# Kernel tuning notes

Measured on AMD Instinct MI355X. Metric: run time of the kernel, lower is better.

The kernel has to match this reference:

```python
import jax, jax.numpy as jnp
import numpy as np


def _segmented_exclusive_cumsum(vals, seg_start_flags):
    """Exclusive cumsum of vals that resets at segment starts (flags True)."""
    def combine(a, b):
        va, fa = a
        vb, fb = b
        return (jnp.where(fb, vb, va + vb), fa | fb)
    inclusive, _ = jax.lax.associative_scan(combine, (vals, seg_start_flags))
    return inclusive - vals


def setup_inputs() -> dict:
    key = jax.random.key(0)
    k1, k2 = jax.random.split(key)
    n_rays = 65536
    samples_per_ray = 128  # average; ragged via sorted random ray ids
    n_pts = n_rays * samples_per_ray  # 8_388_608 sample points
    density = jax.random.normal(k1, (n_pts,), dtype=jnp.float32)
    ray_id = jnp.sort(jax.random.randint(k2, (n_pts,), 0, n_rays)).astype(jnp.int32)
    shift = jnp.float32(-3.0)      # self.act_shift
    interval = jnp.float32(0.5)    # stepsize * voxel_size_ratio
    return {"density": density, "shift": shift, "interval": interval,
            "ray_id": ray_id, "n_rays": n_rays}


def reference(density, shift, interval, ray_id, n_rays):
    # Raw2Alpha: alpha = 1 - exp(-softplus(density + shift) * interval)
    # log(1 - alpha) = -interval * softplus(density + shift)  (stable, no log of tiny)
    log_one_minus_alpha = -interval * jax.nn.softplus(density + shift)
    alpha = 1.0 - jnp.exp(log_one_minus_alpha)

    # Alphas2Weights: per-ray exclusive cumprod of (1 - alpha) in log space.
    # ray_id is sorted; segment starts where the ray id changes.
    seg_start = jnp.concatenate(
        [jnp.ones((1,), dtype=bool), ray_id[1:] != ray_id[:-1]])
    log_T = _segmented_exclusive_cumsum(log_one_minus_alpha, seg_start)
    T = jnp.exp(log_T)                      # transmittance before each sample
    weights = alpha * T                     # [n_pts]

    # alphainv_last[r] = prod over ray r of (1 - alpha) = residual transmittance
    log_total = jax.ops.segment_sum(log_one_minus_alpha, ray_id,
                                    num_segments=n_rays)
    alphainv_last = jnp.exp(log_total)      # [n_rays]; empty rays -> exp(0)=1
    return weights, alphainv_last
```

## Files before the change

kernel.cpp:

```cpp
#include <hip/hip_runtime.h>
#include <math.h>


#define LOG2E 1.4426950408889634f

typedef float vf4 __attribute__((ext_vector_type(4)));

__device__ __forceinline__ float exp2f_(float x) { return __builtin_amdgcn_exp2f(x); }
__device__ __forceinline__ float log2f_(float x) { return __builtin_amdgcn_logf(x); }
__device__ __forceinline__ float rsqf_(float x)  { return __builtin_amdgcn_rsqf(x); }

__device__ __forceinline__ float oma(float d, float sh2, float negc, bool fast) {
    const float y = fmaf(d, LOG2E, sh2);
    if (fast) return rsqf_(1.0f + exp2f_(y));
    const float sp = fmaxf(y, 0.f) + log2f_(1.f + exp2f_(-fabsf(y)));
    return exp2f_(negc * sp);
}

template <int CTRL, int RM>
__device__ __forceinline__ void seg_step(float& V, int& F) {
    const int vs_i = __builtin_amdgcn_update_dpp(
        0x3f800000, __builtin_bit_cast(int, V), CTRL, RM, 0xF, false);
    const int fs = __builtin_amdgcn_update_dpp(0, F, CTRL, RM, 0xF, false);
    const float vs = __builtin_bit_cast(float, vs_i);
    V = F ? V : vs * V;
    F = F | fs;
}

__device__ __forceinline__ float wave_prod_bcast(float x) {
#define STEPP(CTRL, RM)                                                        \
    { int t_ = __builtin_amdgcn_update_dpp(0x3f800000,                         \
          __builtin_bit_cast(int, x), CTRL, RM, 0xF, false);                   \
      x *= __builtin_bit_cast(float, t_); }
    STEPP(0x111, 0xF) STEPP(0x112, 0xF) STEPP(0x114, 0xF)
    STEPP(0x118, 0xF) STEPP(0x142, 0xA) STEPP(0x143, 0xC)
#undef STEPP
    return __builtin_bit_cast(float,
        __builtin_amdgcn_readlane(__builtin_bit_cast(int, x), 63));
}

__device__ __forceinline__ int wave_imax_bcast(int x) {
#define STEPM(CTRL, RM)                                                        \
    { int t_ = __builtin_amdgcn_update_dpp((int)0x80000000, x, CTRL, RM,       \
                                           0xF, false);                        \
      x = (x > t_) ? x : t_; }
    STEPM(0x111, 0xF) STEPM(0x112, 0xF) STEPM(0x114, 0xF)
    STEPM(0x118, 0xF) STEPM(0x142, 0xA) STEPM(0x143, 0xC)
#undef STEPM
    return __builtin_amdgcn_readlane(x, 63);
}

__global__ void __launch_bounds__(256)
fused_alpha_weights(const float* __restrict__ density,
                    const int*   __restrict__ ray_id,
                    const float* __restrict__ shift_p,
                    const float* __restrict__ interval_p,
                    float* __restrict__ weights,
                    float* __restrict__ alphainv,
                    int n_pts, int n_rays) {
    __shared__ float s_wv[4];
    __shared__ int   s_wf[4];
    __shared__ float s_red[4];
    __shared__ int   s_redi[4];

    const int t    = threadIdx.x;
    const int lane = t & 63;
    const int wid  = t >> 6;
    const int base = blockIdx.x << 10;
    const int idx0 = base + t * 4;

    const float shift = shift_p[0];
    const float c     = interval_p[0];
    const float sh2   = shift * LOG2E;
    const float negc  = -c;
    const bool  fast  = (c == 0.5f);

    int r[5]; float d[4];
    bool v0, v1, v2, v3;
    if (idx0 + 4 <= n_pts) {
        const int4   ri = *reinterpret_cast<const int4*>(ray_id + idx0);
        const float4 de = *reinterpret_cast<const float4*>(density + idx0);
        r[0] = ri.x; r[1] = ri.y; r[2] = ri.z; r[3] = ri.w;
        d[0] = de.x; d[1] = de.y; d[2] = de.z; d[3] = de.w;
        v0 = v1 = v2 = v3 = true;
    } else {
        #pragma unroll
        for (int k = 0; k < 4; ++k) {
            const int i = idx0 + k;
            const bool vv = (i < n_pts);
            r[k] = vv ? ray_id[i] : n_rays;
            d[k] = vv ? density[i] : 0.0f;
        }
        v0 = (idx0 < n_pts); v1 = (idx0 + 1 < n_pts);
        v2 = (idx0 + 2 < n_pts); v3 = (idx0 + 3 < n_pts);
    }
    r[4] = (idx0 + 4 < n_pts) ? ray_id[idx0 + 4] : n_rays;
    const int rprev = (idx0 == 0) ? -1
                    : ((idx0 <= n_pts) ? ray_id[idx0 - 1] : n_rays);

    int w_id = 0; float w_den = 0.0f; int rfirst = 0;
    if (base > 0) {
        const int wi = base - 256 + t;
        w_id   = ray_id[wi];
        w_den  = density[wi];
        rfirst = ray_id[base];
    }

    float a0 = oma(d[0], sh2, negc, fast);
    float a1 = oma(d[1], sh2, negc, fast);
    float a2 = oma(d[2], sh2, negc, fast);
    float a3 = oma(d[3], sh2, negc, fast);
    a0 = v0 ? a0 : 1.0f;  a1 = v1 ? a1 : 1.0f;
    a2 = v2 ? a2 : 1.0f;  a3 = v3 ? a3 : 1.0f;

    const int f0 = (r[0] != rprev);
    const int f1 = (r[1] != r[0]);
    const int f2 = (r[2] != r[1]);
    const int f3 = (r[3] != r[2]);

    float V = a0;  int F = f0;
    V = f1 ? a1 : V * a1;  F |= f1;
    V = f2 ? a2 : V * a2;  F |= f2;
    V = f3 ? a3 : V * a3;  F |= f3;

    float Vi = V;  int Fi = F;
    seg_step<0x111, 0xF>(Vi, Fi);
    seg_step<0x112, 0xF>(Vi, Fi);
    seg_step<0x114, 0xF>(Vi, Fi);
    seg_step<0x118, 0xF>(Vi, Fi);
    seg_step<0x142, 0xA>(Vi, Fi);
    seg_step<0x143, 0xC>(Vi, Fi);

    if (lane == 63) { s_wv[wid] = Vi; s_wf[wid] = Fi; }
    if (base > 0) {
        const int cand = (w_id != rfirst) ? t : -1;
        const int wm = wave_imax_bcast(cand);
        if (lane == 0) s_redi[wid] = wm;
    }
    __syncthreads();

    float carry0 = 1.0f;
    if (base > 0) {
        int m = s_redi[0];
        m = (s_redi[1] > m) ? s_redi[1] : m;
        m = (s_redi[2] > m) ? s_redi[2] : m;
        m = (s_redi[3] > m) ? s_redi[3] : m;
        float aa = oma(w_den, sh2, negc, fast);
        if (m >= 0 && t <= m) aa = 1.0f;
        const float wp = wave_prod_bcast(aa);
        if (lane == 0) s_red[wid] = wp;
        __syncthreads();
        carry0 = s_red[0] * s_red[1] * s_red[2] * s_red[3];

        if (m < 0) {
            int lo = base - 256;
            int s0 = -1;
            while (s0 < 0) {
                const int wstart = lo - 256;
                const int i = wstart + t;
                const int vv = (i >= 0) ? ray_id[i] : -1;
                const int c2 = (vv != rfirst) ? t : -1;
                const int wm2 = wave_imax_bcast(c2);
                if (lane == 0) s_redi[wid] = wm2;
                __syncthreads();
                int m2 = s_redi[0];
                m2 = (s_redi[1] > m2) ? s_redi[1] : m2;
                m2 = (s_redi[2] > m2) ? s_redi[2] : m2;
                m2 = (s_redi[3] > m2) ? s_redi[3] : m2;
                __syncthreads();
                if (m2 >= 0) s0 = wstart + m2 + 1; else lo = wstart;
            }
            for (int off = s0; off < base - 256; off += 256) {
                const int i = off + t;
                const float aa2 = (i < base - 256)
                                ? oma(density[i], sh2, negc, fast) : 1.0f;
                const float wp2 = wave_prod_bcast(aa2);
                if (lane == 0) s_red[wid] = wp2;
                __syncthreads();
                carry0 *= s_red[0] * s_red[1] * s_red[2] * s_red[3];
                __syncthreads();
            }
        }
    }

    float Vx = __shfl_up(Vi, 1, 64);
    int   Fx = __shfl_up(Fi, 1, 64);
    if (lane == 0) { Vx = 1.0f; Fx = 0; }

    float Ev = carry0;
    #pragma unroll
    for (int w2 = 0; w2 < 3; ++w2) {
        if (w2 < wid) {
            const float bv = s_wv[w2];  const int bf = s_wf[w2];
            Ev = bf ? bv : Ev * bv;
        }
    }
    Ev = Fx ? Vx : Ev * Vx;

    const float T0 = f0 ? 1.0f : Ev;
    const float e0 = T0 * a0;
    const float T1 = f1 ? 1.0f : e0;
    const float e1 = T1 * a1;
    const float T2 = f2 ? 1.0f : e1;
    const float e2 = T2 * a2;
    const float T3 = f3 ? 1.0f : e2;
    const float e3 = T3 * a3;

    if (idx0 + 4 <= n_pts) {
        vf4 w = { T0 - e0, T1 - e1, T2 - e2, T3 - e3 };
        __builtin_nontemporal_store(w, reinterpret_cast<vf4*>(weights + idx0));
    } else {
        if (v0) weights[idx0]     = T0 - e0;
        if (v1) weights[idx0 + 1] = T1 - e1;
        if (v2) weights[idx0 + 2] = T2 - e2;
        if (v3) weights[idx0 + 3] = T3 - e3;
    }

    if (v0 && r[0] != r[1]) {
        alphainv[r[0]] = e0;
        for (int q = r[0] + 1; q < r[1]; ++q) alphainv[q] = 1.0f;
    }
    if (v1 && r[1] != r[2]) {
        alphainv[r[1]] = e1;
        for (int q = r[1] + 1; q < r[2]; ++q) alphainv[q] = 1.0f;
    }
    if (v2 && r[2] != r[3]) {
        alphainv[r[2]] = e2;
        for (int q = r[2] + 1; q < r[3]; ++q) alphainv[q] = 1.0f;
    }
    if (v3 && r[3] != r[4]) {
        alphainv[r[3]] = e3;
        for (int q = r[3] + 1; q < r[4]; ++q) alphainv[q] = 1.0f;
    }
    if (idx0 == 0) {
        for (int q = 0; q < r[0]; ++q) alphainv[q] = 1.0f;
    }
}

extern "C" void kernel_launch(void* const* d_in, const int* in_sizes, int n_in,
                              void* d_out, int out_size, void* d_ws, size_t ws_size,
                              hipStream_t stream) {
    const float* density  = (const float*)d_in[0];
    const float* shift    = (const float*)d_in[1];
    const float* interval = (const float*)d_in[2];
    const int*   ray_id   = (const int*)d_in[3];
    const int n_pts  = in_sizes[0];
    const int n_rays = out_size - n_pts;

    float* weights  = (float*)d_out;
    float* alphainv = (float*)d_out + n_pts;

    const int grid = (n_pts + 1023) / 1024;
    fused_alpha_weights<<<grid, 256, 0, stream>>>(
        density, ray_id, shift, interval, weights, alphainv, n_pts, n_rays);
}
```

Measured before the change: 24.47 us.

## Process eight points per thread and remap blocks contiguously per XCD

Each thread now handles 8 points instead of 4, using two vectorized loads and stores per array, and the grid shrinks to half as many blocks. This cuts per-block fixed costs: the 256-element lookback window reads, wave scans and shared-memory syncs. Block indices are also remapped so each XCD gets a contiguous range of blocks, meant to keep each block's lookback reads of its neighbour's data in the same L2. The cost is higher register pressure and fewer resident waves for hiding memory latency.

After: 22.73 us. 7.1% less time.

```diff
diff --git a/kernel.cpp b/kernel.cpp
--- a/kernel.cpp
+++ b/kernel.cpp
@@ -3,6 +3,9 @@
 
 
 #define LOG2E 1.4426950408889634f
+#define EPT   8
+#define BPTS  (256 * EPT)
+#define NXCD  8
 
 typedef float vf4 __attribute__((ext_vector_type(4)));
 
@@ -66,8 +69,16 @@
     const int t    = threadIdx.x;
     const int lane = t & 63;
     const int wid  = t >> 6;
-    const int base = blockIdx.x << 10;
-    const int idx0 = base + t * 4;
+
+    const int nwg  = gridDim.x;
+    const int orig = blockIdx.x;
+    const int qq   = nwg / NXCD, rr = nwg % NXCD;
+    const int xcd  = orig % NXCD;
+    const int blk  = (xcd < rr ? xcd * (qq + 1) : rr * (qq + 1) + (xcd - rr) * qq)
+                   + orig / NXCD;
+
+    const int base = blk * BPTS;
+    const int idx0 = base + t * EPT;
 
     const float shift = shift_p[0];
     const float c     = interval_p[0];
@@ -75,26 +86,28 @@
     const float negc  = -c;
     const bool  fast  = (c == 0.5f);
 
-    int r[5]; float d[4];
-    bool v0, v1, v2, v3;
-    if (idx0 + 4 <= n_pts) {
-        const int4   ri = *reinterpret_cast<const int4*>(ray_id + idx0);
-        const float4 de = *reinterpret_cast<const float4*>(density + idx0);
-        r[0] = ri.x; r[1] = ri.y; r[2] = ri.z; r[3] = ri.w;
-        d[0] = de.x; d[1] = de.y; d[2] = de.z; d[3] = de.w;
-        v0 = v1 = v2 = v3 = true;
+    int r[EPT + 1]; float d[EPT]; bool v[EPT];
+    if (idx0 + EPT <= n_pts) {
+        const int4   ri0 = *reinterpret_cast<const int4*>(ray_id + idx0);
+        const int4   ri1 = *reinterpret_cast<const int4*>(ray_id + idx0 + 4);
+        const float4 de0 = *reinterpret_cast<const float4*>(density + idx0);
+        const float4 de1 = *reinterpret_cast<const float4*>(density + idx0 + 4);
+        r[0] = ri0.x; r[1] = ri0.y; r[2] = ri0.z; r[3] = ri0.w;
+        r[4] = ri1.x; r[5] = ri1.y; r[6] = ri1.z; r[7] = ri1.w;
+        d[0] = de0.x; d[1] = de0.y; d[2] = de0.z; d[3] = de0.w;
+        d[4] = de1.x; d[5] = de1.y; d[6] = de1.z; d[7] = de1.w;
+        #pragma unroll
+        for (int k = 0; k < EPT; ++k) v[k] = true;
     } else {
         #pragma unroll
-        for (int k = 0; k < 4; ++k) {
+        for (int k = 0; k < EPT; ++k) {
             const int i = idx0 + k;
-            const bool vv = (i < n_pts);
-            r[k] = vv ? ray_id[i] : n_rays;
-            d[k] = vv ? density[i] : 0.0f;
-        }
-        v0 = (idx0 < n_pts); v1 = (idx0 + 1 < n_pts);
-        v2 = (idx0 + 2 < n_pts); v3 = (idx0 + 3 < n_pts);
-    }
-    r[4] = (idx0 + 4 < n_pts) ? ray_id[idx0 + 4] : n_rays;
+            v[k] = (i < n_pts);
+            r[k] = v[k] ? ray_id[i] : n_rays;
+            d[k] = v[k] ? density[i] : 0.0f;
+        }
+    }
+    r[EPT] = (idx0 + EPT < n_pts) ? ray_id[idx0 + EPT] : n_rays;
     const int rprev = (idx0 == 0) ? -1
                     : ((idx0 <= n_pts) ? ray_id[idx0 - 1] : n_rays);
 
@@ -106,22 +119,20 @@
         rfirst = ray_id[base];
     }
 
-    float a0 = oma(d[0], sh2, negc, fast);
-    float a1 = oma(d[1], sh2, negc, fast);
-    float a2 = oma(d[2], sh2, negc, fast);
-    float a3 = oma(d[3], sh2, negc, fast);
-    a0 = v0 ? a0 : 1.0f;  a1 = v1 ? a1 : 1.0f;
-    a2 = v2 ? a2 : 1.0f;  a3 = v3 ? a3 : 1.0f;
-
-    const int f0 = (r[0] != rprev);
-    const int f1 = (r[1] != r[0]);
-    const int f2 = (r[2] != r[1]);
-    const int f3 = (r[3] != r[2]);
-
-    float V = a0;  int F = f0;
-    V = f1 ? a1 : V * a1;  F |= f1;
-    V = f2 ? a2 : V * a2;  F |= f2;
-    V = f3 ? a3 : V * a3;  F |= f3;
+    float a[EPT]; int f[EPT];
+    #pragma unroll
+    for (int k = 0; k < EPT; ++k) {
+        const float av = oma(d[k], sh2, negc, fast);
+        a[k] = v[k] ? av : 1.0f;
+        f[k] = (k == 0) ? (r[0] != rprev) : (r[k] != r[k - 1]);
+    }
+
+    float V = a[0];  int F = f[0];
+    #pragma unroll
+    for (int k = 1; k < EPT; ++k) {
+        V = f[k] ? a[k] : V * a[k];
+        F |= f[k];
+    }
 
     float Vi = V;  int Fi = F;
     seg_step<0x111, 0xF>(Vi, Fi);
@@ -197,40 +208,32 @@
     }
     Ev = Fx ? Vx : Ev * Vx;
 
-    const float T0 = f0 ? 1.0f : Ev;
-    const float e0 = T0 * a0;
-    const float T1 = f1 ? 1.0f : e0;
-    const float e1 = T1 * a1;
-    const float T2 = f2 ? 1.0f : e1;
-    const float e2 = T2 * a2;
-    const float T3 = f3 ? 1.0f : e2;
-    const float e3 = T3 * a3;
-
-    if (idx0 + 4 <= n_pts) {
-        vf4 w = { T0 - e0, T1 - e1, T2 - e2, T3 - e3 };
-        __builtin_nontemporal_store(w, reinterpret_cast<vf4*>(weights + idx0));
+    float T[EPT], e[EPT];
+    float prev = Ev;
+    #pragma unroll
+    for (int k = 0; k < EPT; ++k) {
+        T[k] = f[k] ? 1.0f : prev;
+        e[k] = T[k] * a[k];
+        prev = e[k];
+    }
+
+    if (idx0 + EPT <= n_pts) {
+        vf4 w0 = { T[0] - e[0], T[1] - e[1], T[2] - e[2], T[3] - e[3] };
+        vf4 w1 = { T[4] - e[4], T[5] - e[5], T[6] - e[6], T[7] - e[7] };
+        __builtin_nontemporal_store(w0, reinterpret_cast<vf4*>(weights + idx0));
+        __builtin_nontemporal_store(w1, reinterpret_cast<vf4*>(weights + idx0 + 4));
     } else {
-        if (v0) weights[idx0]     = T0 - e0;
-        if (v1) weights[idx0 + 1] = T1 - e1;
-        if (v2) weights[idx0 + 2] = T2 - e2;
-        if (v3) weights[idx0 + 3] = T3 - e3;
-    }
-
-    if (v0 && r[0] != r[1]) {
-        alphainv[r[0]] = e0;
-        for (int q = r[0] + 1; q < r[1]; ++q) alphainv[q] = 1.0f;
-    }
-    if (v1 && r[1] != r[2]) {
-        alphainv[r[1]] = e1;
-        for (int q = r[1] + 1; q < r[2]; ++q) alphainv[q] = 1.0f;
-    }
-    if (v2 && r[2] != r[3]) {
-        alphainv[r[2]] = e2;
-        for (int q = r[2] + 1; q < r[3]; ++q) alphainv[q] = 1.0f;
-    }
-    if (v3 && r[3] != r[4]) {
-        alphainv[r[3]] = e3;
-        for (int q = r[3] + 1; q < r[4]; ++q) alphainv[q] = 1.0f;
+        #pragma unroll
+        for (int k = 0; k < EPT; ++k)
+            if (v[k]) weights[idx0 + k] = T[k] - e[k];
+    }
+
+    #pragma unroll
+    for (int k = 0; k < EPT; ++k) {
+        if (v[k] && r[k] != r[k + 1]) {
+            alphainv[r[k]] = e[k];
+            for (int q = r[k] + 1; q < r[k + 1]; ++q) alphainv[q] = 1.0f;
+        }
     }
     if (idx0 == 0) {
         for (int q = 0; q < r[0]; ++q) alphainv[q] = 1.0f;
@@ -250,7 +253,7 @@
     float* weights  = (float*)d_out;
     float* alphainv = (float*)d_out + n_pts;
 
-    const int grid = (n_pts + 1023) / 1024;
+    const int grid = (n_pts + BPTS - 1) / BPTS;
     fused_alpha_weights<<<grid, 256, 0, stream>>>(
         density, ray_id, shift, interval, weights, alphainv, n_pts, n_rays);
 }
```
